# Performance work log

Hardware: AMD Instinct MI355X
Metric: run time of the kernel (lower is better)

## Reference

```python
import jax, jax.numpy as jnp
import numpy as np

NUM_ROUTING = 3
EPS = 1e-8

def squash(s, axis=-1):
    # v = (||s||^2 / (1 + ||s||^2)) * s / ||s||
    n2 = jnp.sum(jnp.square(s), axis=axis, keepdims=True)
    scale = n2 / (1.0 + n2) / jnp.sqrt(n2 + EPS)
    return scale * s

def setup_inputs() -> dict:
    key = jax.random.key(0)
    k1, k2 = jax.random.split(key)
    B, IN_CAPS, IN_DIM = 64, 2048, 16
    NUM_CAPS, DIM = 16, 16
    inputs = jax.random.normal(k1, (B, IN_CAPS, IN_DIM), dtype=jnp.float32)
    # xavier_uniform over last two dims (fan_in=IN_DIM, fan_out=DIM)
    limit = float(np.sqrt(6.0 / (IN_DIM + DIM)))
    W = jax.random.uniform(k2, (IN_CAPS, NUM_CAPS, IN_DIM, DIM), dtype=jnp.float32,
                           minval=-limit, maxval=limit)
    return {"inputs": inputs, "W": W}

def reference(inputs, W):
    # inputs: [B, I, N] ; W: [I, J, N, M] ; inputs_hat: [B, I, J, M]
    inputs_hat = jnp.einsum('ijnm,bin->bijm', W, inputs)
    B, I, J, M = inputs_hat.shape
    b = jnp.zeros((B, I, J), dtype=inputs_hat.dtype)
    outputs = None
    for i in range(NUM_ROUTING):
        c = jax.nn.softmax(b, axis=-1)               # coupling coeffs over output capsules j
        s = jnp.einsum('bij,bijm->bjm', c, inputs_hat)
        outputs = squash(s)                          # [B, J, M]
        if i < NUM_ROUTING - 1:
            b = b + jnp.einsum('bjm,bijm->bij', outputs, inputs_hat)
    return outputs
```

## Files before the change

kernel.cpp:

```cpp
#include <hip/hip_runtime.h>
#include <math.h>

#define BATCH 64
#define IC 2048
#define NI 16
#define NG (IC / NI)
#define NBPB 8
#define NBG (BATCH / NBPB)

template <bool FIRST>
__global__ __launch_bounds__(256, 4) void pass_kernel(
    const float* __restrict__ Wt,
    const float* __restrict__ inp,
    const float* __restrict__ vcum,
    float* __restrict__ partial)
{
    const int tid  = threadIdx.x;
    const int wave = tid >> 6;
    const int lane = tid & 63;
    const int j    = lane & 15;
    const int mg   = lane >> 4;
    const int g    = blockIdx.x & (NG - 1);
    const int bg   = blockIdx.x >> 7;
    const int i0   = g * NI;
    const int bbase = bg * NBPB + wave * 2;

    float4 vc[2];
    if (!FIRST) {
#pragma unroll
        for (int bb = 0; bb < 2; ++bb)
            vc[bb] = *(const float4*)(vcum + (bbase + bb) * 256 + j * 16 + mg * 4);
    }

    float4 acc[2];
    acc[0] = make_float4(0.f, 0.f, 0.f, 0.f);
    acc[1] = make_float4(0.f, 0.f, 0.f, 0.f);

    for (int ii = 0; ii < NI; ++ii) {
        const int i = i0 + ii;
        const float4* wp = (const float4*)(Wt + (size_t)i * 4096 + j * 256 + mg * 4);
        float4 w[16];
#pragma unroll
        for (int n = 0; n < 16; ++n) w[n] = wp[n * 4];

#pragma unroll
        for (int bb = 0; bb < 2; ++bb) {
            const int b = bbase + bb;
            const float4* up = (const float4*)(inp + ((size_t)b * IC + i) * 16);
            float4 u0 = up[0], u1 = up[1], u2 = up[2], u3 = up[3];

            float4 h = make_float4(0.f, 0.f, 0.f, 0.f);
#define ACC4(W, S)                                                     \
            h.x = fmaf((W).x, (S), h.x); h.y = fmaf((W).y, (S), h.y);  \
            h.z = fmaf((W).z, (S), h.z); h.w = fmaf((W).w, (S), h.w);
            ACC4(w[0],  u0.x) ACC4(w[1],  u0.y) ACC4(w[2],  u0.z) ACC4(w[3],  u0.w)
            ACC4(w[4],  u1.x) ACC4(w[5],  u1.y) ACC4(w[6],  u1.z) ACC4(w[7],  u1.w)
            ACC4(w[8],  u2.x) ACC4(w[9],  u2.y) ACC4(w[10], u2.z) ACC4(w[11], u2.w)
            ACC4(w[12], u3.x) ACC4(w[13], u3.y) ACC4(w[14], u3.z) ACC4(w[15], u3.w)
#undef ACC4

            if (FIRST) {
                acc[bb].x += h.x; acc[bb].y += h.y;
                acc[bb].z += h.z; acc[bb].w += h.w;
            } else {
                float t = h.x * vc[bb].x + h.y * vc[bb].y +
                          h.z * vc[bb].z + h.w * vc[bb].w;
                t += __shfl_xor(t, 16);
                t += __shfl_xor(t, 32);
                const float e = __expf(t);
                float s = e;
                s += __shfl_xor(s, 1);
                s += __shfl_xor(s, 2);
                s += __shfl_xor(s, 4);
                s += __shfl_xor(s, 8);
                const float c = e * __builtin_amdgcn_rcpf(s);
                acc[bb].x = fmaf(c, h.x, acc[bb].x);
                acc[bb].y = fmaf(c, h.y, acc[bb].y);
                acc[bb].z = fmaf(c, h.z, acc[bb].z);
                acc[bb].w = fmaf(c, h.w, acc[bb].w);
            }
        }
    }

#pragma unroll
    for (int bb = 0; bb < 2; ++bb)
        *(float4*)(partial + ((size_t)g * BATCH + (bbase + bb)) * 256 + j * 16 + mg * 4) = acc[bb];
}

__global__ __launch_bounds__(256) void reduce_squash(
    const float* __restrict__ partial, float* __restrict__ vcum,
    float* __restrict__ out, int stage)
{
    const int b = blockIdx.x;
    const int tid = threadIdx.x;
    const float* p = partial + (size_t)b * 256 + tid;
    float s = 0.0f;
#pragma unroll 4
    for (int gi = 0; gi < NG; ++gi)
        s += p[(size_t)gi * BATCH * 256];
    if (stage == 0) s *= (1.0f / 16.0f);

    float n2 = s * s;
    n2 += __shfl_xor(n2, 1);
    n2 += __shfl_xor(n2, 2);
    n2 += __shfl_xor(n2, 4);
    n2 += __shfl_xor(n2, 8);
    const float scale = n2 / ((1.0f + n2) * sqrtf(n2 + 1e-8f));
    const float v = scale * s;

    const int o = b * 256 + tid;
    if (stage == 0)      vcum[o] = v;
    else if (stage == 1) vcum[o] += v;
    else                 out[o] = v;
}

extern "C" void kernel_launch(void* const* d_in, const int* in_sizes, int n_in,
                              void* d_out, int out_size, void* d_ws, size_t ws_size,
                              hipStream_t stream) {
    const float* inp = (const float*)d_in[0];
    const float* Wt  = (const float*)d_in[1];
    float* out = (float*)d_out;
    float* partial = (float*)d_ws;
    float* vcum = partial + (size_t)NG * BATCH * 256;

    const dim3 gp(NG * NBG), bp(256);

    pass_kernel<true><<<gp, bp, 0, stream>>>(Wt, inp, nullptr, partial);
    reduce_squash<<<BATCH, 256, 0, stream>>>(partial, vcum, out, 0);
    pass_kernel<false><<<gp, bp, 0, stream>>>(Wt, inp, vcum, partial);
    reduce_squash<<<BATCH, 256, 0, stream>>>(partial, vcum, out, 1);
    pass_kernel<false><<<gp, bp, 0, stream>>>(Wt, inp, vcum, partial);
    reduce_squash<<<BATCH, 256, 0, stream>>>(partial, vcum, out, 2);
}
```

Measured before the change: 487.6 us.

## Reuse W registers across 8 batches per wave and reduce waves in LDS

```diff
diff --git a/kernel.cpp b/kernel.cpp
--- a/kernel.cpp
+++ b/kernel.cpp
@@ -3,13 +3,15 @@
 
 #define BATCH 64
 #define IC 2048
-#define NI 16
-#define NG (IC / NI)
-#define NBPB 8
-#define NBG (BATCH / NBPB)
+#define NIW 8
+#define NW 4
+#define NIB (NIW * NW)
+#define NGB (IC / NIB)
+#define NB 8
+#define NBG (BATCH / NB)
 
 template <bool FIRST>
-__global__ __launch_bounds__(256, 4) void pass_kernel(
+__global__ __launch_bounds__(256, 2) void pass_kernel(
     const float* __restrict__ Wt,
     const float* __restrict__ inp,
     const float* __restrict__ vcum,
@@ -20,33 +22,34 @@
     const int lane = tid & 63;
     const int j    = lane & 15;
     const int mg   = lane >> 4;
-    const int g    = blockIdx.x & (NG - 1);
-    const int bg   = blockIdx.x >> 7;
-    const int i0   = g * NI;
-    const int bbase = bg * NBPB + wave * 2;
+    const int bi = blockIdx.x;
+    const int g  = (bi & 7) | ((bi >> 6) << 3);
+    const int bg = (bi >> 3) & 7;
+    const int i0 = g * NIB + wave * NIW;
+    const int b0 = bg * NB;
 
-    float4 vc[2];
+    float4 vc[NB];
     if (!FIRST) {
 #pragma unroll
-        for (int bb = 0; bb < 2; ++bb)
-            vc[bb] = *(const float4*)(vcum + (bbase + bb) * 256 + j * 16 + mg * 4);
+        for (int b = 0; b < NB; ++b)
+            vc[b] = *(const float4*)(vcum + (b0 + b) * 256 + j * 16 + mg * 4);
     }
 
-    float4 acc[2];
-    acc[0] = make_float4(0.f, 0.f, 0.f, 0.f);
-    acc[1] = make_float4(0.f, 0.f, 0.f, 0.f);
+    float4 acc[NB];
+#pragma unroll
+    for (int b = 0; b < NB; ++b) acc[b] = make_float4(0.f, 0.f, 0.f, 0.f);
 
-    for (int ii = 0; ii < NI; ++ii) {
+    for (int ii = 0; ii < NIW; ++ii) {
         const int i = i0 + ii;
-        const float4* wp = (const float4*)(Wt + (size_t)i * 4096 + j * 256 + mg * 4);
+        const float4* wp = (const float4*)Wt + ((size_t)i * 1024 + j * 64 + mg);
         float4 w[16];
 #pragma unroll
         for (int n = 0; n < 16; ++n) w[n] = wp[n * 4];
 
-#pragma unroll
-        for (int bb = 0; bb < 2; ++bb) {
-            const int b = bbase + bb;
-            const float4* up = (const float4*)(inp + ((size_t)b * IC + i) * 16);
+        const float4* up0 = (const float4*)inp + ((size_t)b0 * IC + i) * 4;
+#pragma unroll 2
+        for (int b = 0; b < NB; ++b) {
+            const float4* up = up0 + (size_t)b * IC * 4;
             float4 u0 = up[0], u1 = up[1], u2 = up[2], u3 = up[3];
 
             float4 h = make_float4(0.f, 0.f, 0.f, 0.f);
@@ -60,11 +63,11 @@
 #undef ACC4
 
             if (FIRST) {
-                acc[bb].x += h.x; acc[bb].y += h.y;
-                acc[bb].z += h.z; acc[bb].w += h.w;
+                acc[b].x += h.x; acc[b].y += h.y;
+                acc[b].z += h.z; acc[b].w += h.w;
             } else {
-                float t = h.x * vc[bb].x + h.y * vc[bb].y +
-                          h.z * vc[bb].z + h.w * vc[bb].w;
+                float t = h.x * vc[b].x + h.y * vc[b].y +
+                          h.z * vc[b].z + h.w * vc[b].w;
                 t += __shfl_xor(t, 16);
                 t += __shfl_xor(t, 32);
                 const float e = __expf(t);
@@ -74,29 +77,46 @@
                 s += __shfl_xor(s, 4);
                 s += __shfl_xor(s, 8);
                 const float c = e * __builtin_amdgcn_rcpf(s);
-                acc[bb].x = fmaf(c, h.x, acc[bb].x);
-                acc[bb].y = fmaf(c, h.y, acc[bb].y);
-                acc[bb].z = fmaf(c, h.z, acc[bb].z);
-                acc[bb].w = fmaf(c, h.w, acc[bb].w);
+                acc[b].x = fmaf(c, h.x, acc[b].x);
+                acc[b].y = fmaf(c, h.y, acc[b].y);
+                acc[b].z = fmaf(c, h.z, acc[b].z);
+                acc[b].w = fmaf(c, h.w, acc[b].w);
             }
         }
     }
 
+    __shared__ float red[NW][NB][256];
 #pragma unroll
-    for (int bb = 0; bb < 2; ++bb)
-        *(float4*)(partial + ((size_t)g * BATCH + (bbase + bb)) * 256 + j * 16 + mg * 4) = acc[bb];
+    for (int b = 0; b < NB; ++b)
+        *(float4*)&red[wave][b][j * 16 + mg * 4] = acc[b];
+    __syncthreads();
+    for (int t = tid; t < NB * 64; t += 256) {
+        const int b  = t >> 6;
+        const int e4 = (t & 63) << 2;
+        float4 r0 = *(const float4*)&red[0][b][e4];
+        float4 r1 = *(const float4*)&red[1][b][e4];
+        float4 r2 = *(const float4*)&red[2][b][e4];
+        float4 r3 = *(const float4*)&red[3][b][e4];
+        float4 s;
+        s.x = (r0.x + r1.x) + (r2.x + r3.x);
+        s.y = (r0.y + r1.y) + (r2.y + r3.y);
+        s.z = (r0.z + r1.z) + (r2.z + r3.z);
+        s.w = (r0.w + r1.w) + (r2.w + r3.w);
+        *(float4*)(partial + ((size_t)g * BATCH + (b0 + b)) * 256 + e4) = s;
+    }
 }
 
-__global__ __launch_bounds__(256) void reduce_squash(
+__global__ __launch_bounds__(64) void reduce_squash(
     const float* __restrict__ partial, float* __restrict__ vcum,
     float* __restrict__ out, int stage)
 {
-    const int b = blockIdx.x;
-    const int tid = threadIdx.x;
-    const float* p = partial + (size_t)b * 256 + tid;
+    const int b = blockIdx.x >> 2;
+    const int q = blockIdx.x & 3;
+    const int e = q * 64 + threadIdx.x;
+    const float* p = partial + (size_t)b * 256 + e;
     float s = 0.0f;
-#pragma unroll 4
-    for (int gi = 0; gi < NG; ++gi)
+#pragma unroll 8
+    for (int gi = 0; gi < NGB; ++gi)
         s += p[(size_t)gi * BATCH * 256];
     if (stage == 0) s *= (1.0f / 16.0f);
 
@@ -108,7 +128,7 @@
     const float scale = n2 / ((1.0f + n2) * sqrtf(n2 + 1e-8f));
     const float v = scale * s;
 
-    const int o = b * 256 + tid;
+    const int o = b * 256 + e;
     if (stage == 0)      vcum[o] = v;
     else if (stage == 1) vcum[o] += v;
     else                 out[o] = v;
@@ -121,14 +141,15 @@
     const float* Wt  = (const float*)d_in[1];
     float* out = (float*)d_out;
     float* partial = (float*)d_ws;
-    float* vcum = partial + (size_t)NG * BATCH * 256;
+    float* vcum = partial + (size_t)NGB * BATCH * 256;
 
-    const dim3 gp(NG * NBG), bp(256);
+    const dim3 gp(NGB * NBG), bp(256);
+    const dim3 gr(BATCH * 4), br(64);
 
     pass_kernel<true><<<gp, bp, 0, stream>>>(Wt, inp, nullptr, partial);
-    reduce_squash<<<BATCH, 256, 0, stream>>>(partial, vcum, out, 0);
+    reduce_squash<<<gr, br, 0, stream>>>(partial, vcum, out, 0);
     pass_kernel<false><<<gp, bp, 0, stream>>>(Wt, inp, vcum, partial);
-    reduce_squash<<<BATCH, 256, 0, stream>>>(partial, vcum, out, 1);
+    reduce_squash<<<gr, br, 0, stream>>>(partial, vcum, out, 1);
     pass_kernel<false><<<gp, bp, 0, stream>>>(Wt, inp, vcum, partial);
-    reduce_squash<<<BATCH, 256, 0, stream>>>(partial, vcum, out, 2);
+    reduce_squash<<<gr, br, 0, stream>>>(partial, vcum, out, 2);
 }
```

After: 453.8 us. -6.9%, faster.
